# Kernel tuning notes

Hardware: AMD Instinct MI355X
Metric: run time of the kernel (lower is better)

## Reference

```python
import jax, jax.numpy as jnp
import numpy as np

B, C, RN, K = 4, 128, 4096, 16
EPS = 1e-5

def _bn_relu(x, gamma, beta):
    # BatchNorm1d in training mode: batch stats over axis 0 (biased var)
    mu = jnp.mean(x, axis=0)
    var = jnp.mean(jnp.square(x - mu), axis=0)
    y = (x - mu) / jnp.sqrt(var + EPS) * gamma + beta
    return jax.nn.relu(y)

def _mlp(x, W, b, gamma, beta):
    return _bn_relu(x @ W.T + b, gamma, beta)

def _knn_idx(pts, k):
    # pts: (B, N, 3) -> (B, N, k) indices of k nearest (incl. self)
    sq = jnp.sum(pts * pts, axis=-1)  # (B, N)
    d2 = sq[:, :, None] + sq[:, None, :] - 2.0 * jnp.einsum('bnd,bmd->bnm', pts, pts)
    _, idx = jax.lax.top_k(-d2, k)
    return idx

def _group(feats, idx):
    # feats: (B, N, C), idx: (B, N, k) -> (B, N, k, C)
    return jax.vmap(lambda f, i: f[i])(feats, idx)

def setup_inputs() -> dict:
    key = jax.random.key(0)
    ks = jax.random.split(key, 16)
    def init_lin(k1, k2, out_c, in_c):
        lim = 1.0 / np.sqrt(in_c)
        W = jax.random.uniform(k1, (out_c, in_c), jnp.float32, -lim, lim)
        b = jax.random.uniform(k2, (out_c,), jnp.float32, -lim, lim)
        return W, b
    W1, b1 = init_lin(ks[0], ks[1], 64, 3)
    W2, b2 = init_lin(ks[2], ks[3], C, C + 64)
    Ww, bw = init_lin(ks[4], ks[5], K, 3)
    return {
        'F_E': jax.random.normal(ks[6], (B, C, RN), jnp.float32),
        'Q_prime': jax.random.normal(ks[7], (B, 3, RN), jnp.float32),
        'W1': W1, 'b1': b1, 'g1': jnp.ones((64,), jnp.float32), 'be1': jnp.zeros((64,), jnp.float32),
        'W2': W2, 'b2': b2, 'g2': jnp.ones((C,), jnp.float32), 'be2': jnp.zeros((C,), jnp.float32),
        'Ww': Ww, 'bw': bw, 'gw': jnp.ones((K,), jnp.float32), 'bew': jnp.zeros((K,), jnp.float32),
    }

def reference(F_E, Q_prime, W1, b1, g1, be1, W2, b2, g2, be2, Ww, bw, gw, bew):
    q = jnp.transpose(Q_prime, (0, 2, 1))   # (B, rN, 3)
    f = jnp.transpose(F_E, (0, 2, 1))       # (B, rN, C)
    idx = _knn_idx(q, K)                     # (B, rN, K)
    grouped_Q = _group(q, idx)               # (B, rN, K, 3)
    grouped_F = _group(f, idx)               # (B, rN, K, C)
    sub_Q = grouped_Q - q[:, :, None, :]     # (B, rN, K, 3)
    sub_flat = sub_Q.reshape(-1, 3)
    enc_sub = _mlp(sub_flat, W1, b1, g1, be1).reshape(B, RN, K, 64)
    concat = jnp.concatenate([grouped_F, enc_sub], axis=-1).reshape(-1, C + 64)
    enc_feat = _mlp(concat, W2, b2, g2, be2).reshape(B, RN, K, C)
    sw = _mlp(sub_flat, Ww, bw, gw, bew).reshape(B, RN, K, K)
    # einsum 'brkc,brkk->brkc' takes the diagonal of sw over its last two axes
    w_diag = jnp.diagonal(sw, axis1=2, axis2=3)  # (B, rN, K)
    weighted = jnp.sum(enc_feat * w_diag[..., None], axis=2)  # (B, rN, C)
    refined = weighted + f
    return jnp.transpose(refined, (0, 2, 1))
```

## Files before the change

### kernel.cpp

```cpp
#include <hip/hip_runtime.h>
#include <hip/hip_bf16.h>

#define BB 4
#define CC 128
#define RN 4096
#define KK 16
#define NROWS (BB*RN*KK)
#define EPSV 1e-5f

typedef __attribute__((ext_vector_type(8))) short short8;
typedef __attribute__((ext_vector_type(4))) float f32x4;

__device__ inline ushort f2bf(float f) {
    union { __hip_bfloat16 h; ushort u; } cv;
    cv.h = __float2bfloat16(f);
    return cv.u;
}

__device__ inline float readlane_f(float v, int src) {
    return __uint_as_float((uint)__builtin_amdgcn_readlane((int)__float_as_uint(v), src));
}


__global__ void k_prep(const float* __restrict__ Q, float4* __restrict__ qp,
                       const float* __restrict__ W2, ushort* __restrict__ W2b) {
    int blk = blockIdx.x;
    if (blk < 64) {
        int gid = blk * 256 + threadIdx.x;
        int b = gid >> 12, n = gid & (RN - 1);
        size_t base = (size_t)b * 3 * RN;
        float x = Q[base + n], y = Q[base + RN + n], z = Q[base + 2 * RN + n];
        qp[gid] = make_float4(x, y, z, fmaf(x, x, fmaf(y, y, z * z)));
    } else {
        int i = (blk - 64) * 256 + threadIdx.x;
        if (i < 128 * 192) W2b[i] = f2bf(W2[i]);
    }
}

__global__ void k_transpose(const float* __restrict__ FE, ushort* __restrict__ ftb) {
    __shared__ float t[32][33];
    int bid = blockIdx.x;
    int b = bid >> 9;
    int cb = (bid >> 7) & 3;
    int nb = bid & 127;
    int c0 = cb * 32, n0 = nb * 32;
    int tid = threadIdx.x;
    for (int o = tid; o < 1024; o += 256) {
        int i = o >> 5, j = o & 31;
        t[i][j] = FE[((size_t)b * CC + c0 + i) * RN + n0 + j];
    }
    __syncthreads();
    for (int o = tid; o < 512; o += 256) {
        int j = o >> 4, i2 = (o & 15) * 2;
        uint p = (uint)f2bf(t[i2][j]) | ((uint)f2bf(t[i2 + 1][j]) << 16);
        *(uint*)(ftb + ((size_t)(b * RN + n0 + j) * 128 + c0 + i2)) = p;
    }
}

__global__ __launch_bounds__(256) void k_knn(const float4* __restrict__ qp, int* __restrict__ idxout,
                                             float* __restrict__ zwout, float* __restrict__ statslots,
                                             const float* __restrict__ Ww, const float* __restrict__ bw) {
    __shared__ float bacc[9];
    const int tid = threadIdx.x;
    if (tid < 9) bacc[tid] = 0.f;
    __syncthreads();
    const int lane = tid & 63;
    const int wid = tid >> 6;
    const int row = blockIdx.x * 4 + wid;
    const int b = row >> 12, n = row & (RN - 1);
    const float4* qb = qp + b * RN;
    const float4 self = qb[n];
    const int upaddr = ((lane - 1) & 63) << 2;

    float ld; int li;
    {
        float4 cp = qb[lane];
        ld = self.w + cp.w - 2.f * fmaf(self.x, cp.x, fmaf(self.y, cp.y, self.z * cp.z));
        li = lane;
        #pragma unroll
        for (int k = 2; k <= 64; k <<= 1) {
            #pragma unroll
            for (int j = k >> 1; j > 0; j >>= 1) {
                float od = __shfl_xor(ld, j);
                int   oi = __shfl_xor(li, j);
                bool up    = ((lane & k) == 0);
                bool lower = ((lane & j) == 0);
                bool myless = (ld < od) || (ld == od && li < oi);
                bool keep = (myless == lower) == up;
                if (!keep) { ld = od; li = oi; }
            }
        }
    }
    float g15d = readlane_f(ld, 15);
    int   g15i = __builtin_amdgcn_readlane(li, 15);

    float4 cur = qb[64 + lane];
    for (int t0 = 64; t0 < RN; t0 += 64) {
        float4 nxt = qb[t0 + 64 + lane];
        const float d2 = self.w + cur.w - 2.f * fmaf(self.x, cur.x, fmaf(self.y, cur.y, self.z * cur.z));
        bool beats = (d2 < g15d) || (d2 == g15d && (t0 + lane) < g15i);
        unsigned long long mask = __ballot(beats);
        if (mask) {
            do {
                float sd = __uint_as_float((uint)__builtin_amdgcn_ds_bpermute(upaddr, (int)__float_as_uint(ld)));
                int   si = __builtin_amdgcn_ds_bpermute(upaddr, li);
                int src = (int)__builtin_ctzll(mask);
                mask &= mask - 1;
                float cd = readlane_f(d2, src);
                int   ci = t0 + src;
                bool lt2 = (ld < cd) || (ld == cd && li < ci);
                int p = (int)__builtin_popcountll(__ballot(lt2) & 0xFFFFull);
                if (lane == p)      { ld = cd; li = ci; }
                else if (lane > p)  { ld = sd; li = si; }
            } while (mask);
            g15d = readlane_f(ld, 15);
            g15i = __builtin_amdgcn_readlane(li, 15);
        }
        cur = nxt;
    }

    float sx = 0.f, sy = 0.f, sz = 0.f;
    if (lane < 16) {
        idxout[row * 16 + lane] = li;
        float4 pn = qb[li];
        sx = pn.x - self.x; sy = pn.y - self.y; sz = pn.z - self.z;
        float zw = fmaf(Ww[lane * 3], sx, fmaf(Ww[lane * 3 + 1], sy, fmaf(Ww[lane * 3 + 2], sz, bw[lane])));
        zwout[row * 16 + lane] = zw;
    }
    float vals[9] = {sx, sy, sz, sx * sx, sx * sy, sx * sz, sy * sy, sy * sz, sz * sz};
    #pragma unroll
    for (int i = 0; i < 9; ++i) {
        float v = vals[i];
        for (int off = 32; off; off >>= 1) v += __shfl_down(v, off);
        if (lane == 0) atomicAdd(&bacc[i], v);
    }
    __syncthreads();
    if (tid < 9) atomicAdd(&statslots[(blockIdx.x & 63) * 12 + tid], bacc[tid]);
}

__global__ void k_bn1(const float* __restrict__ slots, const float* __restrict__ W1, const float* __restrict__ b1,
                      const float* __restrict__ g1, const float* __restrict__ be1,
                      const float* __restrict__ Ww, const float* __restrict__ bw,
                      const float* __restrict__ gw, const float* __restrict__ bew, float* __restrict__ par) {
    __shared__ float st[12];
    int tid = threadIdx.x;
    if (tid < 12) {
        float s = 0.f;
        for (int i = 0; i < 64; ++i) s += slots[i * 12 + tid];
        st[tid] = s;
    }
    __syncthreads();
    const float invN = 1.0f / (float)NROWS;
    float mx = st[0] * invN, my = st[1] * invN, mz = st[2] * invN;
    float Cxx = st[3] * invN - mx * mx, Cxy = st[4] * invN - mx * my, Cxz = st[5] * invN - mx * mz;
    float Cyy = st[6] * invN - my * my, Cyz = st[7] * invN - my * mz, Czz = st[8] * invN - mz * mz;
    if (tid < 64) {
        float w0 = W1[tid * 3], w1 = W1[tid * 3 + 1], w2 = W1[tid * 3 + 2];
        float mean = w0 * mx + w1 * my + w2 * mz + b1[tid];
        float var = w0 * w0 * Cxx + w1 * w1 * Cyy + w2 * w2 * Czz
                  + 2.f * (w0 * w1 * Cxy + w0 * w2 * Cxz + w1 * w2 * Cyz);
        float sc = g1[tid] * rsqrtf(var + EPSV);
        par[tid] = sc;
        par[64 + tid] = be1[tid] - mean * sc;
    } else if (tid < 80) {
        int k = tid - 64;
        float w0 = Ww[k * 3], w1 = Ww[k * 3 + 1], w2 = Ww[k * 3 + 2];
        float mean = w0 * mx + w1 * my + w2 * mz + bw[k];
        float var = w0 * w0 * Cxx + w1 * w1 * Cyy + w2 * w2 * Czz
                  + 2.f * (w0 * w1 * Cxy + w0 * w2 * Cxz + w1 * w2 * Cyz);
        float sc = gw[k] * rsqrtf(var + EPSV);
        par[128 + k] = sc;
        par[144 + k] = bew[k] - mean * sc;
    }
}

__global__ __launch_bounds__(256) void k_main(const ushort* __restrict__ ftb, const int* __restrict__ idxb,
                                              const float4* __restrict__ qp, const float* __restrict__ W1,
                                              const float* __restrict__ b1, const ushort* __restrict__ W2b,
                                              const float* __restrict__ b2, const float* __restrict__ par,
                                              float* __restrict__ bn2slots, __hip_bfloat16* __restrict__ z2) {
    __shared__ ushort A_lds[64][200];
    __shared__ float subs[64][3];
    __shared__ int nbr[64];
    const int tid = threadIdx.x;
    const int bid = blockIdx.x;
    const int pair0 = bid * 4;
    const int b = pair0 >> 12;

    if (tid < 64) {
        int g = tid >> 4, k = tid & 15;
        int pair = pair0 + g;
        int n = idxb[pair * 16 + k];
        nbr[tid] = n;
        float4 pn = qp[b * RN + n];
        float4 ps = qp[pair];
        subs[tid][0] = pn.x - ps.x;
        subs[tid][1] = pn.y - ps.y;
        subs[tid][2] = pn.z - ps.z;
    }
    __syncthreads();
    for (int o = tid; o < 1024; o += 256) {
        int r = o >> 4, c8 = (o & 15) * 8;
        const ushort* src = ftb + ((size_t)(b * RN + nbr[r]) * 128 + c8);
        *(short8*)&A_lds[r][c8] = *(const short8*)src;
    }
    for (int o = tid; o < 2048; o += 256) {
        int r = o >> 5, c2 = (o & 31) * 2;
        float z0 = fmaf(W1[c2 * 3],     subs[r][0], fmaf(W1[c2 * 3 + 1], subs[r][1], fmaf(W1[c2 * 3 + 2], subs[r][2], b1[c2])));
        float z1 = fmaf(W1[c2 * 3 + 3], subs[r][0], fmaf(W1[c2 * 3 + 4], subs[r][1], fmaf(W1[c2 * 3 + 5], subs[r][2], b1[c2 + 1])));
        float e0 = fmaxf(fmaf(z0, par[c2],     par[64 + c2]),     0.f);
        float e1 = fmaxf(fmaf(z1, par[c2 + 1], par[64 + c2 + 1]), 0.f);
        *(uint*)&A_lds[r][128 + c2] = (uint)f2bf(e0) | ((uint)f2bf(e1) << 16);
    }
    __syncthreads();

    const int lane = tid & 63, w = tid >> 6;
    const int lr = lane & 15, lg = lane >> 4;
    const int cbase = w * 32;

    short8 af[12];
    #pragma unroll
    for (int ct = 0; ct < 2; ++ct)
        #pragma unroll
        for (int kt = 0; kt < 6; ++kt)
            af[ct * 6 + kt] = *(const short8*)(W2b + (size_t)(cbase + ct * 16 + lr) * 192 + kt * 32 + lg * 8);

    float4 b2v[2];
    b2v[0] = *(const float4*)&b2[cbase + lg * 4];
    b2v[1] = *(const float4*)&b2[cbase + 16 + lg * 4];

    float st_s[8], st_q[8];
    #pragma unroll
    for (int i = 0; i < 8; ++i) { st_s[i] = 0.f; st_q[i] = 0.f; }

    #pragma unroll
    for (int nt = 0; nt < 4; ++nt) {
        short8 bf[6];
        #pragma unroll
        for (int kt = 0; kt < 6; ++kt)
            bf[kt] = *(const short8*)&A_lds[nt * 16 + lr][kt * 32 + lg * 8];
        #pragma unroll
        for (int ct = 0; ct < 2; ++ct) {
            f32x4 acc = {0.f, 0.f, 0.f, 0.f};
            #pragma unroll
            for (int kt = 0; kt < 6; ++kt)
                acc = __builtin_amdgcn_mfma_f32_16x16x32_bf16(af[ct * 6 + kt], bf[kt], acc, 0, 0, 0);
            const int c0 = cbase + ct * 16 + lg * 4;
            const size_t row = (size_t)pair0 * 16 + nt * 16 + lr;
            union { __hip_bfloat16 h[4]; uint2 u2; } pk;
            const float4 bb = b2v[ct];
            float vb[4] = {bb.x, bb.y, bb.z, bb.w};
            #pragma unroll
            for (int cc = 0; cc < 4; ++cc) {
                float v = acc[cc] + vb[cc];
                st_s[ct * 4 + cc] += v;
                st_q[ct * 4 + cc] = fmaf(v, v, st_q[ct * 4 + cc]);
                pk.h[cc] = __float2bfloat16(v);
            }
            *(uint2*)(z2 + row * CC + c0) = pk.u2;
        }
    }
    #pragma unroll
    for (int i = 0; i < 8; ++i) {
        float s = st_s[i], q = st_q[i];
        #pragma unroll
        for (int m = 1; m < 16; m <<= 1) { s += __shfl_xor(s, m); q += __shfl_xor(q, m); }
        if (lr == 0) {
            int ct = i >> 2, cc = i & 3;
            int c = cbase + ct * 16 + lg * 4 + cc;
            atomicAdd(&bn2slots[(bid & 63) * 256 + c * 2], s);
            atomicAdd(&bn2slots[(bid & 63) * 256 + c * 2 + 1], q);
        }
    }
}

__global__ void k_bn2(const float* __restrict__ slots, const float* __restrict__ g2,
                      const float* __restrict__ be2, float* __restrict__ par) {
    __shared__ float red[256];
    int tid = threadIdx.x;
    float v = 0.f;
    for (int s = 0; s < 64; ++s) v += slots[s * 256 + tid];
    red[tid] = v;
    __syncthreads();
    if (tid < 128) {
        const float invN = 1.0f / (float)NROWS;
        float mean = red[2 * tid] * invN;
        float var = red[2 * tid + 1] * invN - mean * mean;
        float sc = g2[tid] * rsqrtf(var + EPSV);
        par[160 + tid] = sc;
        par[288 + tid] = be2[tid] - mean * sc;
    }
}

__global__ __launch_bounds__(256) void k_out(const __hip_bfloat16* __restrict__ z2, const float* __restrict__ zw_raw,
                                             const float* __restrict__ par, const float* __restrict__ F_E,
                                             float* __restrict__ out) {
    __shared__ float wd[32][16];
    __shared__ float outs[32][129];
    const int tid = threadIdx.x;
    const int b = blockIdx.x >> 7;
    const int r0 = (blockIdx.x & 127) * 32;
    const int rowbase = (b * RN + r0) * 16;
    for (int o = tid; o < 512; o += 256) {
        int rr = o >> 4, k = o & 15;
        wd[rr][k] = fmaxf(fmaf(zw_raw[rowbase + o], par[128 + k], par[144 + k]), 0.f);
    }
    __syncthreads();
    const int c0 = (tid & 63) * 2;
    const int rh = tid >> 6;
    const float sc0 = par[160 + c0], sh0 = par[288 + c0];
    const float sc1 = par[160 + c0 + 1], sh1 = par[288 + c0 + 1];
    for (int rr = rh; rr < 32; rr += 4) {
        float a0 = 0.f, a1 = 0.f;
        const __hip_bfloat16* zp = z2 + ((size_t)rowbase + rr * 16) * CC + c0;
        #pragma unroll
        for (int k = 0; k < 16; ++k) {
            unsigned int uu = *(const unsigned int*)(zp + k * CC);
            float z0 = __uint_as_float(uu << 16);
            float z1 = __uint_as_float(uu & 0xFFFF0000u);
            float w = wd[rr][k];
            a0 += fmaxf(fmaf(z0, sc0, sh0), 0.f) * w;
            a1 += fmaxf(fmaf(z1, sc1, sh1), 0.f) * w;
        }
        outs[rr][c0] = a0; outs[rr][c0 + 1] = a1;
    }
    __syncthreads();
    for (int o = tid; o < 4096; o += 256) {
        int c = o >> 5, rr = o & 31;
        size_t oi = ((size_t)b * CC + c) * RN + r0 + rr;
        out[oi] = outs[rr][c] + F_E[oi];
    }
}

extern "C" void kernel_launch(void* const* d_in, const int* in_sizes, int n_in,
                              void* d_out, int out_size, void* d_ws, size_t ws_size,
                              hipStream_t stream) {
    const float* F_E = (const float*)d_in[0];
    const float* Qp  = (const float*)d_in[1];
    const float* W1  = (const float*)d_in[2];
    const float* b1  = (const float*)d_in[3];
    const float* g1  = (const float*)d_in[4];
    const float* be1 = (const float*)d_in[5];
    const float* W2  = (const float*)d_in[6];
    const float* b2  = (const float*)d_in[7];
    const float* g2  = (const float*)d_in[8];
    const float* be2 = (const float*)d_in[9];
    const float* Ww  = (const float*)d_in[10];
    const float* bw  = (const float*)d_in[11];
    const float* gw  = (const float*)d_in[12];
    const float* bew = (const float*)d_in[13];
    float* out = (float*)d_out;
    float* wsf = (float*)d_ws;

    float* bn2slots   = wsf;
    float* statslots  = wsf + 16384;
    float* par        = wsf + 17152;
    ushort* W2b       = (ushort*)(wsf + 17664);
    float4* qpack     = (float4*)(wsf + 32768);
    int* idxb         = (int*)(wsf + 98304);
    float* zw_raw     = wsf + 360448;
    ushort* ftb       = (ushort*)(wsf + 622592);
    __hip_bfloat16* z2 = (__hip_bfloat16*)(wsf + 1671168);

    hipMemsetAsync(d_ws, 0, 17152 * sizeof(float), stream);
    k_prep<<<160, 256, 0, stream>>>(Qp, qpack, W2, W2b);
    k_transpose<<<2048, 256, 0, stream>>>(F_E, ftb);
    k_knn<<<4096, 256, 0, stream>>>(qpack, idxb, zw_raw, statslots, Ww, bw);
    k_bn1<<<1, 128, 0, stream>>>(statslots, W1, b1, g1, be1, Ww, bw, gw, bew, par);
    k_main<<<4096, 256, 0, stream>>>(ftb, idxb, qpack, W1, b1, W2b, b2, par, bn2slots, z2);
    k_bn2<<<1, 256, 0, stream>>>(bn2slots, g2, be2, par);
    k_out<<<512, 256, 0, stream>>>(z2, zw_raw, par, F_E, out);
}
```

Before: 254.8 us.

## Load gathered features straight to registers, stage z2 stores through LDS, swizzle tiles

The gathered neighbor feature rows now load directly from global memory into MFMA B-operand registers instead of going through LDS, so only the encoded-position part is staged in shared memory. The LDS buffer is reused as a union to transpose the bf16 outputs, turning scattered 8-byte z2 stores into coalesced 16-byte row stores. Block IDs are remapped so consecutive blocks spread across batches or XCDs. This trades extra syncs and higher register pressure for fewer LDS round trips and better global write coalescing.

```diff
diff --git a/kernel.cpp b/kernel.cpp
--- a/kernel.cpp
+++ b/kernel.cpp
@@ -179,51 +179,59 @@
                                               const float* __restrict__ b1, const ushort* __restrict__ W2b,
                                               const float* __restrict__ b2, const float* __restrict__ par,
                                               float* __restrict__ bn2slots, __hip_bfloat16* __restrict__ z2) {
-    __shared__ ushort A_lds[64][200];
+    __shared__ union {
+        ushort enc[64][72];
+        ushort z2s[64][132];
+    } u;
     __shared__ float subs[64][3];
     __shared__ int nbr[64];
     const int tid = threadIdx.x;
-    const int bid = blockIdx.x;
-    const int pair0 = bid * 4;
+    const int tile = ((blockIdx.x & 7) << 9) | (blockIdx.x >> 3);
+    const int pair0 = tile * 4;
     const int b = pair0 >> 12;
-
-    if (tid < 64) {
-        int g = tid >> 4, k = tid & 15;
-        int pair = pair0 + g;
-        int n = idxb[pair * 16 + k];
-        nbr[tid] = n;
+    const int lane = tid & 63, w = tid >> 6;
+    const int lr = lane & 15, lg = lane >> 4;
+
+    if (lane < 16) {
+        int pair = pair0 + w;
+        int n = idxb[pair * 16 + lane];
+        int r = w * 16 + lane;
+        nbr[r] = n;
         float4 pn = qp[b * RN + n];
         float4 ps = qp[pair];
-        subs[tid][0] = pn.x - ps.x;
-        subs[tid][1] = pn.y - ps.y;
-        subs[tid][2] = pn.z - ps.z;
-    }
-    __syncthreads();
-    for (int o = tid; o < 1024; o += 256) {
-        int r = o >> 4, c8 = (o & 15) * 8;
-        const ushort* src = ftb + ((size_t)(b * RN + nbr[r]) * 128 + c8);
-        *(short8*)&A_lds[r][c8] = *(const short8*)src;
-    }
+        subs[r][0] = pn.x - ps.x;
+        subs[r][1] = pn.y - ps.y;
+        subs[r][2] = pn.z - ps.z;
+    }
+    __syncthreads();
+
+    short8 bfg[4][4];
+    #pragma unroll
+    for (int nt = 0; nt < 4; ++nt) {
+        const ushort* fr = ftb + ((size_t)(b * RN + nbr[nt * 16 + lr]) * 128) + lg * 8;
+        bfg[nt][0] = *(const short8*)(fr);
+        bfg[nt][1] = *(const short8*)(fr + 32);
+        bfg[nt][2] = *(const short8*)(fr + 64);
+        bfg[nt][3] = *(const short8*)(fr + 96);
+    }
+
+    const int cbase = w * 32;
+    short8 af[12];
+    #pragma unroll
+    for (int ct = 0; ct < 2; ++ct)
+        #pragma unroll
+        for (int kt = 0; kt < 6; ++kt)
+            af[ct * 6 + kt] = *(const short8*)(W2b + (size_t)(cbase + ct * 16 + lr) * 192 + kt * 32 + lg * 8);
+
     for (int o = tid; o < 2048; o += 256) {
         int r = o >> 5, c2 = (o & 31) * 2;
         float z0 = fmaf(W1[c2 * 3],     subs[r][0], fmaf(W1[c2 * 3 + 1], subs[r][1], fmaf(W1[c2 * 3 + 2], subs[r][2], b1[c2])));
         float z1 = fmaf(W1[c2 * 3 + 3], subs[r][0], fmaf(W1[c2 * 3 + 4], subs[r][1], fmaf(W1[c2 * 3 + 5], subs[r][2], b1[c2 + 1])));
         float e0 = fmaxf(fmaf(z0, par[c2],     par[64 + c2]),     0.f);
         float e1 = fmaxf(fmaf(z1, par[c2 + 1], par[64 + c2 + 1]), 0.f);
-        *(uint*)&A_lds[r][128 + c2] = (uint)f2bf(e0) | ((uint)f2bf(e1) << 16);
-    }
-    __syncthreads();
-
-    const int lane = tid & 63, w = tid >> 6;
-    const int lr = lane & 15, lg = lane >> 4;
-    const int cbase = w * 32;
-
-    short8 af[12];
-    #pragma unroll
-    for (int ct = 0; ct < 2; ++ct)
-        #pragma unroll
-        for (int kt = 0; kt < 6; ++kt)
-            af[ct * 6 + kt] = *(const short8*)(W2b + (size_t)(cbase + ct * 16 + lr) * 192 + kt * 32 + lg * 8);
+        *(uint*)&u.enc[r][c2] = (uint)f2bf(e0) | ((uint)f2bf(e1) << 16);
+    }
+    __syncthreads();
 
     float4 b2v[2];
     b2v[0] = *(const float4*)&b2[cbase + lg * 4];
@@ -233,31 +241,54 @@
     #pragma unroll
     for (int i = 0; i < 8; ++i) { st_s[i] = 0.f; st_q[i] = 0.f; }
 
+    float accs[4][2][4];
     #pragma unroll
     for (int nt = 0; nt < 4; ++nt) {
-        short8 bf[6];
-        #pragma unroll
-        for (int kt = 0; kt < 6; ++kt)
-            bf[kt] = *(const short8*)&A_lds[nt * 16 + lr][kt * 32 + lg * 8];
+        const int r = nt * 16 + lr;
+        short8 be0 = *(const short8*)&u.enc[r][lg * 8];
+        short8 be1 = *(const short8*)&u.enc[r][32 + lg * 8];
         #pragma unroll
         for (int ct = 0; ct < 2; ++ct) {
             f32x4 acc = {0.f, 0.f, 0.f, 0.f};
-            #pragma unroll
-            for (int kt = 0; kt < 6; ++kt)
-                acc = __builtin_amdgcn_mfma_f32_16x16x32_bf16(af[ct * 6 + kt], bf[kt], acc, 0, 0, 0);
-            const int c0 = cbase + ct * 16 + lg * 4;
-            const size_t row = (size_t)pair0 * 16 + nt * 16 + lr;
-            union { __hip_bfloat16 h[4]; uint2 u2; } pk;
+            acc = __builtin_amdgcn_mfma_f32_16x16x32_bf16(af[ct * 6 + 0], bfg[nt][0], acc, 0, 0, 0);
+            acc = __builtin_amdgcn_mfma_f32_16x16x32_bf16(af[ct * 6 + 1], bfg[nt][1], acc, 0, 0, 0);
+            acc = __builtin_amdgcn_mfma_f32_16x16x32_bf16(af[ct * 6 + 2], bfg[nt][2], acc, 0, 0, 0);
+            acc = __builtin_amdgcn_mfma_f32_16x16x32_bf16(af[ct * 6 + 3], bfg[nt][3], acc, 0, 0, 0);
+            acc = __builtin_amdgcn_mfma_f32_16x16x32_bf16(af[ct * 6 + 4], be0, acc, 0, 0, 0);
+            acc = __builtin_amdgcn_mfma_f32_16x16x32_bf16(af[ct * 6 + 5], be1, acc, 0, 0, 0);
             const float4 bb = b2v[ct];
             float vb[4] = {bb.x, bb.y, bb.z, bb.w};
             #pragma unroll
             for (int cc = 0; cc < 4; ++cc) {
                 float v = acc[cc] + vb[cc];
+                accs[nt][ct][cc] = v;
                 st_s[ct * 4 + cc] += v;
                 st_q[ct * 4 + cc] = fmaf(v, v, st_q[ct * 4 + cc]);
-                pk.h[cc] = __float2bfloat16(v);
             }
-            *(uint2*)(z2 + row * CC + c0) = pk.u2;
+        }
+    }
+    __syncthreads();
+
+    #pragma unroll
+    for (int nt = 0; nt < 4; ++nt) {
+        #pragma unroll
+        for (int ct = 0; ct < 2; ++ct) {
+            union { __hip_bfloat16 h[4]; uint2 u2; } pk;
+            #pragma unroll
+            for (int cc = 0; cc < 4; ++cc) pk.h[cc] = __float2bfloat16(accs[nt][ct][cc]);
+            *(uint2*)&u.z2s[nt * 16 + lr][cbase + ct * 16 + lg * 4] = pk.u2;
+        }
+    }
+    __syncthreads();
+    {
+        __hip_bfloat16* zbase = z2 + (size_t)pair0 * 16 * CC;
+        #pragma unroll
+        for (int p = 0; p < 4; ++p) {
+            int e = p * 256 + tid;
+            int row = e >> 4, unit = e & 15;
+            uint2 v0 = *(uint2*)&u.z2s[row][unit * 8];
+            uint2 v1 = *(((uint2*)&u.z2s[row][unit * 8]) + 1);
+            *(uint4*)(zbase + (size_t)row * CC + unit * 8) = make_uint4(v0.x, v0.y, v1.x, v1.y);
         }
     }
     #pragma unroll
@@ -268,8 +299,8 @@
         if (lr == 0) {
             int ct = i >> 2, cc = i & 3;
             int c = cbase + ct * 16 + lg * 4 + cc;
-            atomicAdd(&bn2slots[(bid & 63) * 256 + c * 2], s);
-            atomicAdd(&bn2slots[(bid & 63) * 256 + c * 2 + 1], q);
+            atomicAdd(&bn2slots[(tile & 63) * 256 + c * 2], s);
+            atomicAdd(&bn2slots[(tile & 63) * 256 + c * 2 + 1], q);
         }
     }
 }
```

Result: slower. 273.1 us (+7.2%).
